# Performance work log

Hardware: AMD Instinct MI355X
Metric: run time of the kernel (lower is better)

Reference implementation:

```python
import jax, jax.numpy as jnp
import numpy as np

B, H, GRID_H, GRID_W, C = 8, 16, 64, 64, 128
R = C // 4  # N_RDIM: rotary pair dim per axis
N = GRID_H * GRID_W


def _make_cs(max_pos, r):
    # RoPE cos/sin table: [max_pos, r, 2] with cos at [...,0], sin at [...,1]
    inv_freq = 1.0 / (10000.0 ** (jnp.arange(r, dtype=jnp.float32) / r))
    ang = jnp.arange(max_pos, dtype=jnp.float32)[:, None] * inv_freq[None, :]
    return jnp.stack([jnp.cos(ang), jnp.sin(ang)], axis=-1)


def setup_inputs() -> dict:
    key = jax.random.key(0)
    kx, = jax.random.split(key, 1)
    x = jax.random.normal(kx, (B, H, N, C), dtype=jnp.float32)
    # packed indices: (row << 16) | col, as in encode_idx
    rows = jnp.arange(GRID_H, dtype=jnp.int32)
    cols = jnp.arange(GRID_W, dtype=jnp.int32)
    idx = ((rows[:, None] << 16) | cols[None, :]).reshape(-1).astype(jnp.int32)
    row_cs = _make_cs(GRID_H, R)
    col_cs = _make_cs(GRID_W, R)
    return {"x": x, "idx": idx, "row_cs": row_cs, "col_cs": col_cs}


def reference(x, idx, row_cs, col_cs):
    r = row_cs.shape[1]
    row = (idx >> 16).astype(jnp.int32)      # [N]
    col = (idx & 0xFFFF).astype(jnp.int32)   # [N]
    rc = row_cs[row]                          # [N, R, 2] gathered per token
    cc = col_cs[col]                          # [N, R, 2]
    rcos, rsin = rc[..., 0], rc[..., 1]       # [N, R]
    ccos, csin = cc[..., 0], cc[..., 1]
    x0 = x[..., 0:r]
    x1 = x[..., r:2 * r]
    x2 = x[..., 2 * r:3 * r]
    x3 = x[..., 3 * r:4 * r]
    # row rotation on first half, col rotation on second half
    y0 = x0 * rcos - x1 * rsin
    y1 = x0 * rsin + x1 * rcos
    y2 = x2 * ccos - x3 * csin
    y3 = x2 * csin + x3 * ccos
    return jnp.concatenate([y0, y1, y2, y3], axis=-1)
```

## Files before the change

kernel.cpp:

```cpp
#include <hip/hip_runtime.h>


#define NPOS 4096
#define F4_PER_ROW 32

__global__ __launch_bounds__(256)
void rope2d_kernel(const float4* __restrict__ x,
                   const int*    __restrict__ idx,
                   const float4* __restrict__ row_cs,
                   const float4* __restrict__ col_cs,
                   float4*       __restrict__ out,
                   long long total)
{
    const long long stride = (long long)gridDim.x * blockDim.x;
    for (long long g = (long long)blockIdx.x * blockDim.x + threadIdx.x;
         g < total; g += stride) {
        const long long rowid = g >> 3;
        const int t = (int)(g & 7);
        const int n = (int)(rowid & (NPOS - 1));

        const int id   = idx[n];
        const int prow = id >> 16;
        const int pcol = id & 0xffff;

        const long long base = rowid * F4_PER_ROW;

        const float4 x0 = x[base + t];
        const float4 x1 = x[base + t + 8];
        const float4 x2 = x[base + t + 16];
        const float4 x3 = x[base + t + 24];

        const float4 rcs0 = row_cs[prow * 16 + t * 2];
        const float4 rcs1 = row_cs[prow * 16 + t * 2 + 1];
        const float4 ccs0 = col_cs[pcol * 16 + t * 2];
        const float4 ccs1 = col_cs[pcol * 16 + t * 2 + 1];

        float4 y0, y1, y2, y3;
        y0.x = x0.x * rcs0.x - x1.x * rcs0.y;   y1.x = x0.x * rcs0.y + x1.x * rcs0.x;
        y0.y = x0.y * rcs0.z - x1.y * rcs0.w;   y1.y = x0.y * rcs0.w + x1.y * rcs0.z;
        y0.z = x0.z * rcs1.x - x1.z * rcs1.y;   y1.z = x0.z * rcs1.y + x1.z * rcs1.x;
        y0.w = x0.w * rcs1.z - x1.w * rcs1.w;   y1.w = x0.w * rcs1.w + x1.w * rcs1.z;

        y2.x = x2.x * ccs0.x - x3.x * ccs0.y;   y3.x = x2.x * ccs0.y + x3.x * ccs0.x;
        y2.y = x2.y * ccs0.z - x3.y * ccs0.w;   y3.y = x2.y * ccs0.w + x3.y * ccs0.z;
        y2.z = x2.z * ccs1.x - x3.z * ccs1.y;   y3.z = x2.z * ccs1.y + x3.z * ccs1.x;
        y2.w = x2.w * ccs1.z - x3.w * ccs1.w;   y3.w = x2.w * ccs1.w + x3.w * ccs1.z;

        out[base + t]      = y0;
        out[base + t + 8]  = y1;
        out[base + t + 16] = y2;
        out[base + t + 24] = y3;
    }
}

extern "C" void kernel_launch(void* const* d_in, const int* in_sizes, int n_in,
                              void* d_out, int out_size, void* d_ws, size_t ws_size,
                              hipStream_t stream) {
    const float4* x      = (const float4*)d_in[0];
    const int*    idx    = (const int*)d_in[1];
    const float4* row_cs = (const float4*)d_in[2];
    const float4* col_cs = (const float4*)d_in[3];
    float4*       out    = (float4*)d_out;

    const long long total = (long long)in_sizes[0] / 16;

    const int block = 256;
    long long want = (total + block - 1) / block;
    int grid = (int)(want < 2048 ? want : 2048);

    rope2d_kernel<<<grid, block, 0, stream>>>(x, idx, row_cs, col_cs, out, total);
}
```

Measured before the change: 100.0 us.

## Reuse gathered cos/sin across 16 batch-head slices per thread

Each thread now loads the idx entry and its row/col cos-sin values once, then loops over 16 batch-head slices, applying them to each. The old grid-stride loop over all elements is replaced by a fixed grid of 1024 blocks with no bounds check. This is meant to cut the redundant idx and table gathers and the 64-bit index math per element. In exchange the code hard-codes B*H=128 and N=4096 and assumes the input size matches exactly.

```diff
diff --git a/kernel.cpp b/kernel.cpp
--- a/kernel.cpp
+++ b/kernel.cpp
@@ -3,37 +3,40 @@
 
 #define NPOS 4096
 #define F4_PER_ROW 32
+#define BH 128
+#define BH_PER_THREAD 16
+#define NCHUNK (BH / BH_PER_THREAD)
 
 __global__ __launch_bounds__(256)
 void rope2d_kernel(const float4* __restrict__ x,
                    const int*    __restrict__ idx,
                    const float4* __restrict__ row_cs,
                    const float4* __restrict__ col_cs,
-                   float4*       __restrict__ out,
-                   long long total)
+                   float4*       __restrict__ out)
 {
-    const long long stride = (long long)gridDim.x * blockDim.x;
-    for (long long g = (long long)blockIdx.x * blockDim.x + threadIdx.x;
-         g < total; g += stride) {
-        const long long rowid = g >> 3;
-        const int t = (int)(g & 7);
-        const int n = (int)(rowid & (NPOS - 1));
+    const int g = blockIdx.x * 256 + threadIdx.x;
+    const int t     = g & 7;
+    const int n     = (g >> 3) & (NPOS - 1);
+    const int chunk = g >> 15;
 
-        const int id   = idx[n];
-        const int prow = id >> 16;
-        const int pcol = id & 0xffff;
+    const int id   = idx[n];
+    const int prow = id >> 16;
+    const int pcol = id & 0xffff;
 
-        const long long base = rowid * F4_PER_ROW;
+    const float4 rcs0 = row_cs[prow * 16 + t * 2];
+    const float4 rcs1 = row_cs[prow * 16 + t * 2 + 1];
+    const float4 ccs0 = col_cs[pcol * 16 + t * 2];
+    const float4 ccs1 = col_cs[pcol * 16 + t * 2 + 1];
 
-        const float4 x0 = x[base + t];
-        const float4 x1 = x[base + t + 8];
-        const float4 x2 = x[base + t + 16];
-        const float4 x3 = x[base + t + 24];
+    long long base = ((long long)(chunk * BH_PER_THREAD) * NPOS + n) * F4_PER_ROW + t;
+    const long long step = (long long)NPOS * F4_PER_ROW;
 
-        const float4 rcs0 = row_cs[prow * 16 + t * 2];
-        const float4 rcs1 = row_cs[prow * 16 + t * 2 + 1];
-        const float4 ccs0 = col_cs[pcol * 16 + t * 2];
-        const float4 ccs1 = col_cs[pcol * 16 + t * 2 + 1];
+    #pragma unroll 4
+    for (int i = 0; i < BH_PER_THREAD; ++i, base += step) {
+        const float4 x0 = x[base];
+        const float4 x1 = x[base + 8];
+        const float4 x2 = x[base + 16];
+        const float4 x3 = x[base + 24];
 
         float4 y0, y1, y2, y3;
         y0.x = x0.x * rcs0.x - x1.x * rcs0.y;   y1.x = x0.x * rcs0.y + x1.x * rcs0.x;
@@ -46,10 +49,10 @@
         y2.z = x2.z * ccs1.x - x3.z * ccs1.y;   y3.z = x2.z * ccs1.y + x3.z * ccs1.x;
         y2.w = x2.w * ccs1.z - x3.w * ccs1.w;   y3.w = x2.w * ccs1.w + x3.w * ccs1.z;
 
-        out[base + t]      = y0;
-        out[base + t + 8]  = y1;
-        out[base + t + 16] = y2;
-        out[base + t + 24] = y3;
+        out[base]      = y0;
+        out[base + 8]  = y1;
+        out[base + 16] = y2;
+        out[base + 24] = y3;
     }
 }
 
@@ -62,11 +65,9 @@
     const float4* col_cs = (const float4*)d_in[3];
     float4*       out    = (float4*)d_out;
 
-    const long long total = (long long)in_sizes[0] / 16;
+    const int work_items = NCHUNK * NPOS * 8;
+    const int block = 256;
+    const int grid = work_items / block;
 
-    const int block = 256;
-    long long want = (total + block - 1) / block;
-    int grid = (int)(want < 2048 ? want : 2048);
-
-    rope2d_kernel<<<grid, block, 0, stream>>>(x, idx, row_cs, col_cs, out, total);
+    rope2d_kernel<<<grid, block, 0, stream>>>(x, idx, row_cs, col_cs, out);
 }
```

Measured after the change: 106.3 us. +6.3%, slower.
